# Kernel optimization log

Hardware: AMD Instinct MI355X
Metric: run time of the kernel (lower is better)

## Reference

```python
import jax, jax.numpy as jnp
import numpy as np

# dims
B, S, V, H, D, I, L, SL, P = 1, 2048, 32000, 1024, 512, 4096, 2, 32, 4096
DECAY_FAST, DECAY_SLOW, CONS_RATE, CONS_EVERY = 0.9, 0.99, 0.1, 10


def _ln(x, g, b):
    m = x.mean(-1, keepdims=True)
    v = ((x - m) ** 2).mean(-1, keepdims=True)
    return (x - m) * jax.lax.rsqrt(v + 1e-5) * g + b


def _memory_scan(items, gates, fast0, slow0):
    # items [B,S,D], gates [B,S,SL]; sequential per-timestep memory update
    cons = (jnp.arange(items.shape[1]) % CONS_EVERY) == 0
    def step(carry, x):
        fast, slow = carry
        item, gate, c = x
        fast = DECAY_FAST * fast + gate[:, :, None] * item[:, None, :]
        slow = jnp.where(c, DECAY_SLOW * slow + CONS_RATE * fast, slow)
        fast = jnp.where(c, (1.0 - CONS_RATE) * fast, fast)
        return (fast, slow), None
    (fast, slow), _ = jax.lax.scan(
        step, (fast0, slow0),
        (items.transpose(1, 0, 2), gates.transpose(1, 0, 2), cons))
    return fast, slow


def _forward(input_ids, fast_states, slow_states, emb, pos_emb, W_item, b_item,
             W_q, b_q, rh_W1, rh_b1, rh_W2, rh_b2, gate_W, gate_b, W_out, b_out,
             ln1_g, ln1_b, ffn_W1, ffn_b1, ffn_W2, ffn_b2, ln2_g, ln2_b, fln_g, fln_b):
    b, s = input_ids.shape
    h = emb[input_ids] + pos_emb[:s][None]  # [B,S,H]
    new_fast, new_slow = [], []
    for l in range(W_item.shape[0]):
        items = h @ W_item[l] + b_item[l]          # [B,S,D]
        query = h @ W_q[l] + b_q[l]                # [B,S,H]
        # retrieval head -> unit-norm unbinding keys
        k1 = jax.nn.gelu(items @ rh_W1[l] + rh_b1[l])
        keys = k1 @ rh_W2[l] + rh_b2[l]
        keys = keys / (jnp.linalg.norm(keys, axis=-1, keepdims=True) + 1e-6)
        fast0, slow0 = fast_states[l], slow_states[l]  # [B,SL,D]
        # retrieval uses the initial (constant-within-sequence) states, so it
        # vectorizes over seq: slot attention + hadamard unbinding
        mem = jnp.concatenate([fast0, slow0], axis=1)  # [B,2*SL,D]
        scores = jnp.einsum('bsd,bnd->bsn', keys, mem) / jnp.sqrt(jnp.float32(D))
        attn = jax.nn.softmax(scores, axis=-1)
        retrieved = jnp.einsum('bsn,bnd->bsd', attn, mem) * keys  # [B,S,D]
        gates = jax.nn.sigmoid(jnp.concatenate([h, retrieved], -1) @ gate_W[l] + gate_b[l])
        fast_gates = gates[..., :SL]
        fast, slow = _memory_scan(items, fast_gates, fast0, slow0)
        new_fast.append(fast)
        new_slow.append(slow)
        out = jnp.concatenate([query, retrieved], -1) @ W_out[l] + b_out[l]
        h = _ln(h + out, ln1_g[l], ln1_b[l])
        ffn = jax.nn.gelu(h @ ffn_W1[l] + ffn_b1[l]) @ ffn_W2[l] + ffn_b2[l]
        h = _ln(h + ffn, ln2_g[l], ln2_b[l])
    h = _ln(h, fln_g, fln_b)
    logits = jnp.einsum('bsh,vh->bsv', h, emb)  # tied lm_head
    return logits, jnp.stack(new_fast), jnp.stack(new_slow)


def setup_inputs() -> dict:
    key = jax.random.key(0)
    def rn(i, shape, scale=0.02):
        return jax.random.normal(jax.random.fold_in(key, i), shape, dtype=jnp.float32) * scale
    z = lambda shape: jnp.zeros(shape, jnp.float32)
    return dict(
        input_ids=jax.random.randint(jax.random.fold_in(key, 0), (B, S), 0, V),
        fast_states=rn(100, (L, B, SL, D), 0.5),
        slow_states=rn(101, (L, B, SL, D), 0.5),
        emb=rn(1, (V, H)),
        pos_emb=rn(2, (P, H)),
        W_item=rn(3, (L, H, D)), b_item=z((L, D)),
        W_q=rn(4, (L, H, H)), b_q=z((L, H)),
        rh_W1=rn(5, (L, D, 2 * D)), rh_b1=z((L, 2 * D)),
        rh_W2=rn(6, (L, 2 * D, D)), rh_b2=z((L, D)),
        gate_W=rn(7, (L, H + D, 2 * SL)), gate_b=z((L, 2 * SL)),
        W_out=rn(8, (L, H + D, H)), b_out=z((L, H)),
        ln1_g=jnp.ones((L, H)), ln1_b=z((L, H)),
        ffn_W1=rn(9, (L, H, I)), ffn_b1=z((L, I)),
        ffn_W2=rn(10, (L, I, H)), ffn_b2=z((L, H)),
        ln2_g=jnp.ones((L, H)), ln2_b=z((L, H)),
        fln_g=jnp.ones((H,)), fln_b=z((H,)),
    )


def reference(input_ids, fast_states, slow_states, emb, pos_emb, W_item, b_item,
              W_q, b_q, rh_W1, rh_b1, rh_W2, rh_b2, gate_W, gate_b, W_out, b_out,
              ln1_g, ln1_b, ffn_W1, ffn_b1, ffn_W2, ffn_b2, ln2_g, ln2_b, fln_g, fln_b):
    return _forward(input_ids, fast_states, slow_states, emb, pos_emb, W_item, b_item,
                    W_q, b_q, rh_W1, rh_b1, rh_W2, rh_b2, gate_W, gate_b, W_out, b_out,
                    ln1_g, ln1_b, ffn_W1, ffn_b1, ffn_W2, ffn_b2, ln2_g, ln2_b, fln_g, fln_b)
```

## Files before the change

### kernel.cpp

```cpp
#include <hip/hip_runtime.h>
#include <hip/hip_bf16.h>
#include <stdint.h>

typedef __hip_bfloat16 bf16;
typedef float f32x4 __attribute__((ext_vector_type(4)));
typedef short s16x8 __attribute__((ext_vector_type(8)));
typedef short s16x4 __attribute__((ext_vector_type(4)));

#define DEV __device__ __forceinline__

static constexpr int S_ = 2048, H_ = 1024, D_ = 512, I_ = 4096, V_ = 32000;
static constexpr int SLn = 32, Lc = 2;
static constexpr size_t LOGITS_N = (size_t)S_ * V_;

DEV float gelu_f(float x) {
    float x3 = x * x * x;
    return 0.5f * x * (1.f + tanhf(0.7978845608028654f * (x + 0.044715f * x3)));
}

#define AS1(p) ((const __attribute__((address_space(1))) void*)(uintptr_t)(p))
#define AS3(p) ((__attribute__((address_space(3))) void*)(uint32_t)(uintptr_t)(p))

__global__ __launch_bounds__(256, 2) void logits_gemm(const bf16* __restrict__ A,
                                                      const bf16* __restrict__ BT,
                                                      float* __restrict__ C) {
    constexpr int NT = 32, SLOT = 128 * 32;
    __shared__ short lds[4 * SLOT];
    const int tid = threadIdx.x, lane = tid & 63;
    const int wm = (tid >> 6) >> 1, wn = (tid >> 6) & 1;

    int bid = blockIdx.x;
    int wgid = (bid & 7) * 250 + (bid >> 3);
    const int m0 = (wgid & 7) * 256;
    const int n0 = (wgid >> 3) * 128;

    const bf16* bS[2];
#pragma unroll
    for (int c = 0; c < 2; ++c) {
        int L = (c * 256 + tid) * 16;
        int sidx = L >> 10, w = L & 1023;
        int r16 = w >> 6;
        int c2 = (w & 63) ^ (((r16 >> 3) & 1) << 5);
        bS[c] = BT + (size_t)(n0 + sidx * 16 + r16) * 1024 + (c2 >> 1);
    }
    auto stageB = [&](int kt) {
        short* dst = &lds[(kt & 3) * SLOT];
#pragma unroll
        for (int c = 0; c < 2; ++c)
            __builtin_amdgcn_global_load_lds(AS1(bS[c] + kt * 32), AS3(dst + (c * 256 + tid) * 8), 16, 0, 0);
    };
    const int laneoff = ((lane & 15) * 64 + ((((lane >> 4) * 8) ^ (((lane >> 3) & 1) << 4)) << 1)) >> 1;

    const bf16* aP[8];
#pragma unroll
    for (int fi = 0; fi < 8; ++fi)
        aP[fi] = A + (size_t)(m0 + wm * 128 + fi * 16 + (lane & 15)) * 1536 + ((lane >> 4) * 8);

    f32x4 acc[8][4];
#pragma unroll
    for (int i = 0; i < 8; i++)
#pragma unroll
        for (int j = 0; j < 4; j++)
#pragma unroll
            for (int r = 0; r < 4; r++) acc[i][j][r] = 0.f;

    s16x8 a0[8], a1[8];
    stageB(0);
    stageB(1);
    stageB(2);
#pragma unroll
    for (int fi = 0; fi < 8; ++fi) a0[fi] = *(const s16x8*)(aP[fi]);
    asm volatile("s_waitcnt vmcnt(0)" ::: "memory");
    __builtin_amdgcn_s_barrier();

    auto iter = [&](int t, s16x8(&cur)[8], s16x8(&nxt)[8]) {
        const short* bs = &lds[(t & 3) * SLOT];
        s16x8 bf[4];
#pragma unroll
        for (int j = 0; j < 4; ++j)
            bf[j] = *(const s16x8*)&bs[(wn * 4 + j) * 512 + laneoff];
        if (t + 1 < NT) {
#pragma unroll
            for (int fi = 0; fi < 8; ++fi) nxt[fi] = *(const s16x8*)(aP[fi] + (t + 1) * 32);
        }
        if (t >= 1 && t + 2 < NT) stageB(t + 2);
        if (t + 2 < NT)
            asm volatile("s_waitcnt vmcnt(10)" ::: "memory");
        else if (t + 1 < NT)
            asm volatile("s_waitcnt vmcnt(8)" ::: "memory");
        else
            asm volatile("s_waitcnt vmcnt(0)" ::: "memory");
        asm volatile("s_waitcnt lgkmcnt(0)" ::: "memory");
        __builtin_amdgcn_s_barrier();
        __builtin_amdgcn_sched_barrier(0);
        __builtin_amdgcn_s_setprio(1);
#pragma unroll
        for (int i = 0; i < 8; ++i)
#pragma unroll
            for (int j = 0; j < 4; ++j)
                acc[i][j] = __builtin_amdgcn_mfma_f32_16x16x32_bf16(cur[i], bf[j], acc[i][j], 0, 0, 0);
        __builtin_amdgcn_s_setprio(0);
    };

    for (int t = 0; t < NT; t += 2) {
        iter(t, a0, a1);
        iter(t + 1, a1, a0);
    }

#pragma unroll
    for (int i = 0; i < 8; i++) {
        int gr0 = m0 + (wm * 8 + i) * 16 + ((lane >> 4) << 2);
#pragma unroll
        for (int j = 0; j < 4; j++) {
            int gc = n0 + (wn * 4 + j) * 16 + (lane & 15);
#pragma unroll
            for (int r = 0; r < 4; r++) C[(size_t)(gr0 + r) * V_ + gc] = acc[i][j][r];
        }
    }
}

template <int BM, int BN, int TH, int WM, int WN, int FLAGS>
__global__ __launch_bounds__(TH, 3) void gemm_p5(
    const bf16* __restrict__ A, int lda, const bf16* __restrict__ BT,
    const float* __restrict__ bias, const float* __restrict__ bias2,
    float* __restrict__ Cf, int ldf, bf16* __restrict__ Cb, int ldb2,
    bf16* __restrict__ Cb2, int K, int Mt, int Nt) {
    constexpr int FM = BM / (WM * 16), FN = BN / (WN * 16);
    constexpr int CA = (BM * 4) / TH, CB = (BN * 4) / TH, CH = CA + CB;
    constexpr int NPH = (FM * FN >= 32) ? 2 : 1;
    constexpr int FMP = FM / NPH;
    constexpr int BUFS = (BM + BN) * 32;
    __shared__ short lds[4 * BUFS];
    const int tid = threadIdx.x, lane = tid & 63;
    const int wm = (tid >> 6) / WN, wn = (tid >> 6) % WN;

    int nwg = Mt * Nt;
    int bid = blockIdx.x, wgid = bid;
    if ((nwg & 7) == 0) {
        int cpx = nwg >> 3;
        wgid = (bid & 7) * cpx + (bid >> 3);
    }
    const int m0 = (wgid % Mt) * BM, n0 = (wgid / Mt) * BN;

    const bf16* aS[CA];
    const bf16* bS[CB];
#pragma unroll
    for (int c = 0; c < CA; ++c) {
        int L = (c * TH + tid) * 16;
        int sidx = L >> 10, w = L & 1023;
        int r16 = w >> 6;
        int c2 = (w & 63) ^ (((r16 >> 3) & 1) << 5);
        aS[c] = A + (size_t)(m0 + sidx * 16 + r16) * lda + (c2 >> 1);
    }
#pragma unroll
    for (int c = 0; c < CB; ++c) {
        int L = (c * TH + tid) * 16;
        int sidx = L >> 10, w = L & 1023;
        int r16 = w >> 6;
        int c2 = (w & 63) ^ (((r16 >> 3) & 1) << 5);
        bS[c] = BT + (size_t)(n0 + sidx * 16 + r16) * K + (c2 >> 1);
    }

    auto stageA = [&](int kt) {
        short* dst = &lds[(kt & 3) * BUFS];
#pragma unroll
        for (int c = 0; c < CA; ++c)
            __builtin_amdgcn_global_load_lds(AS1(aS[c] + kt * 32), AS3(dst + (c * TH + tid) * 8), 16, 0, 0);
    };
    auto stageB = [&](int kt) {
        short* dst = &lds[(kt & 3) * BUFS + BM * 32];
#pragma unroll
        for (int c = 0; c < CB; ++c)
            __builtin_amdgcn_global_load_lds(AS1(bS[c] + kt * 32), AS3(dst + (c * TH + tid) * 8), 16, 0, 0);
    };

    const int laneoff = ((lane & 15) * 64 + ((((lane >> 4) * 8) ^ (((lane >> 3) & 1) << 4)) << 1)) >> 1;

    f32x4 acc[FM][FN];
#pragma unroll
    for (int i = 0; i < FM; i++)
#pragma unroll
        for (int j = 0; j < FN; j++)
#pragma unroll
            for (int r = 0; r < 4; r++) acc[i][j][r] = 0.f;

    const int NT = K >> 5;
    stageA(0); stageB(0);
    stageA(1); stageB(1);
    stageA(2); stageB(2);
    asm volatile("s_waitcnt vmcnt(%0)" ::"n"(2 * CH) : "memory");
    __builtin_amdgcn_s_barrier();
    for (int t = 0; t < NT; ++t) {
        const short* as = &lds[(t & 3) * BUFS];
        const short* bs = as + BM * 32;
        s16x8 bf[FN];
#pragma unroll
        for (int p = 0; p < NPH; ++p) {
            s16x8 af[FMP];
#pragma unroll
            for (int i = 0; i < FMP; i++)
                af[i] = *(const s16x8*)&as[(wm * FM + p * FMP + i) * 512 + laneoff];
            if (p == 0) {
#pragma unroll
                for (int j = 0; j < FN; j++)
                    bf[j] = *(const s16x8*)&bs[(wn * FN + j) * 512 + laneoff];
            }
            if (t + 3 < NT) {
                if (NPH == 1) {
                    stageA(t + 3);
                    stageB(t + 3);
                } else if (p == 0) {
                    stageA(t + 3);
                } else {
                    stageB(t + 3);
                }
            }
            if (p == NPH - 1) {
                const int rem = NT - 1 - t;
                if (rem >= 3)
                    asm volatile("s_waitcnt vmcnt(%0)" ::"n"(2 * CH) : "memory");
                else if (rem == 2)
                    asm volatile("s_waitcnt vmcnt(%0)" ::"n"(CH) : "memory");
                else
                    asm volatile("s_waitcnt vmcnt(0)" ::: "memory");
            }
            __builtin_amdgcn_s_barrier();
            __builtin_amdgcn_sched_barrier(0);
            __builtin_amdgcn_s_setprio(1);
#pragma unroll
            for (int i = 0; i < FMP; i++)
#pragma unroll
                for (int j = 0; j < FN; j++)
                    acc[p * FMP + i][j] =
                        __builtin_amdgcn_mfma_f32_16x16x32_bf16(af[i], bf[j], acc[p * FMP + i][j], 0, 0, 0);
            __builtin_amdgcn_s_setprio(0);
            __builtin_amdgcn_s_barrier();
        }
    }

#pragma unroll
    for (int i = 0; i < FM; i++) {
        int gr0 = m0 + (wm * FM + i) * 16 + ((lane >> 4) << 2);
#pragma unroll
        for (int j = 0; j < FN; j++) {
            int gc = n0 + (wn * FN + j) * 16 + (lane & 15);
            if (FLAGS & 32) {
                if (n0 < 512) {
                    float bv = bias[gc];
#pragma unroll
                    for (int r = 0; r < 4; r++) {
                        float v = acc[i][j][r] + bv;
                        Cf[(size_t)(gr0 + r) * 512 + gc] = v;
                        Cb2[(size_t)(gr0 + r) * 512 + gc] = __float2bfloat16(v);
                    }
                } else {
                    float bv = bias2[gc - 512];
#pragma unroll
                    for (int r = 0; r < 4; r++)
                        Cb[(size_t)(gr0 + r) * 1536 + (gc - 512)] = __float2bfloat16(acc[i][j][r] + bv);
                }
            } else {
                float bv = (FLAGS & 1) ? bias[gc] : 0.f;
#pragma unroll
                for (int r = 0; r < 4; r++) {
                    float v = acc[i][j][r] + bv;
                    if (FLAGS & 2) v = gelu_f(v);
                    if (FLAGS & 4) Cf[(size_t)(gr0 + r) * ldf + gc] = v;
                    if (FLAGS & 8) Cb[(size_t)(gr0 + r) * ldb2 + gc] = __float2bfloat16(v);
                }
            }
        }
    }
}

__global__ __launch_bounds__(256) void transpose_bf16_kernel(const float* __restrict__ W,
                                                             bf16* __restrict__ WT, int K, int N) {
    __shared__ float t[32][33];
    int tx = threadIdx.x & 31, ty = threadIdx.x >> 5;
    int kb = blockIdx.y * 32, nb = blockIdx.x * 32;
#pragma unroll
    for (int i = 0; i < 4; i++)
        t[ty + 8 * i][tx] = W[(size_t)(kb + ty + 8 * i) * N + nb + tx];
    __syncthreads();
#pragma unroll
    for (int i = 0; i < 4; i++)
        WT[(size_t)(nb + ty + 8 * i) * K + kb + tx] = __float2bfloat16(t[tx][ty + 8 * i]);
}

__global__ void conv_bf16_kernel(const float* __restrict__ src, bf16* __restrict__ dst) {
    size_t i = (size_t)blockIdx.x * 256 + threadIdx.x;
    f32x4 v = ((const f32x4*)src)[i];
    s16x4 o;
#pragma unroll
    for (int j = 0; j < 4; j++) {
        bf16 h = __float2bfloat16(v[j]);
        o[j] = *(short*)&h;
    }
    ((s16x4*)dst)[i] = o;
}

__global__ void embed_kernel(const int* __restrict__ ids, const float* __restrict__ emb,
                             const float* __restrict__ pos, float* __restrict__ hF,
                             bf16* __restrict__ hB) {
    int t = blockIdx.x, tid = threadIdx.x;
    int id = ids[t];
    f32x4 v = ((const f32x4*)(emb + (size_t)id * H_))[tid];
    f32x4 q = ((const f32x4*)(pos + (size_t)t * H_))[tid];
    v = v + q;
    ((f32x4*)(hF + (size_t)t * H_))[tid] = v;
    s16x4 o;
#pragma unroll
    for (int j = 0; j < 4; j++) {
        bf16 h = __float2bfloat16(v[j]);
        o[j] = *(short*)&h;
    }
    ((s16x4*)(hB + (size_t)t * 1536))[tid] = o;
}

__global__ __launch_bounds__(256) void ln_kernel(const float* __restrict__ x,
                                                 const float* __restrict__ res,
                                                 const float* __restrict__ g,
                                                 const float* __restrict__ b,
                                                 float* __restrict__ of, bf16* __restrict__ ob,
                                                 int ldo) {
    __shared__ float red[8];
    int row = blockIdx.x, tid = threadIdx.x, lane = tid & 63, wid = tid >> 6;
    const float* xr = x + (size_t)row * H_;
    float v[4];
#pragma unroll
    for (int j = 0; j < 4; j++) {
        int c = tid + 256 * j;
        v[j] = xr[c] + (res ? res[(size_t)row * H_ + c] : 0.f);
    }
    float s = v[0] + v[1] + v[2] + v[3];
#pragma unroll
    for (int o = 32; o; o >>= 1) s += __shfl_xor(s, o);
    if (!lane) red[wid] = s;
    __syncthreads();
    float mean = (red[0] + red[1] + red[2] + red[3]) * (1.f / H_);
    float q = 0.f;
#pragma unroll
    for (int j = 0; j < 4; j++) {
        float d = v[j] - mean;
        q += d * d;
    }
#pragma unroll
    for (int o = 32; o; o >>= 1) q += __shfl_xor(q, o);
    if (!lane) red[4 + wid] = q;
    __syncthreads();
    float var = (red[4] + red[5] + red[6] + red[7]) * (1.f / H_);
    float rstd = rsqrtf(var + 1e-5f);
#pragma unroll
    for (int j = 0; j < 4; j++) {
        int c = tid + 256 * j;
        float o2 = (v[j] - mean) * rstd * g[c] + b[c];
        if (of) of[(size_t)row * H_ + c] = o2;
        if (ob) ob[(size_t)row * ldo + c] = __float2bfloat16(o2);
    }
}

__global__ void memt_kernel(const float* __restrict__ fast0, const float* __restrict__ slow0,
                            float* __restrict__ memT) {
    int idx = blockIdx.x * 256 + threadIdx.x;
    int d = idx >> 6, n = idx & 63;
    const float* m = (n < 32) ? fast0 + (size_t)n * D_ : slow0 + (size_t)(n - 32) * D_;
    memT[idx] = m[d];
}

__global__ __launch_bounds__(256) void attn_kernel(const float* __restrict__ keys,
                                                   const float* __restrict__ memT,
                                                   const float* __restrict__ fast0,
                                                   const float* __restrict__ slow0,
                                                   bf16* __restrict__ qr, bf16* __restrict__ hr) {
    __shared__ float klds[4][512];
    int wid = threadIdx.x >> 6, lane = threadIdx.x & 63;
    int r = blockIdx.x * 4 + wid;
    float kv[8], ss = 0.f;
#pragma unroll
    for (int j = 0; j < 8; j++) {
        kv[j] = keys[(size_t)r * D_ + lane + 64 * j];
        ss += kv[j] * kv[j];
    }
#pragma unroll
    for (int o = 32; o; o >>= 1) ss += __shfl_xor(ss, o);
    float inv = 1.f / (sqrtf(ss) + 1e-6f);
#pragma unroll
    for (int j = 0; j < 8; j++) {
        kv[j] *= inv;
        klds[wid][lane + 64 * j] = kv[j];
    }
    __syncthreads();
    float s0 = 0.f, s1 = 0.f, s2 = 0.f, s3 = 0.f;
#pragma unroll 8
    for (int d = 0; d < 512; d += 4) {
        s0 = fmaf(klds[wid][d + 0], memT[(d + 0) * 64 + lane], s0);
        s1 = fmaf(klds[wid][d + 1], memT[(d + 1) * 64 + lane], s1);
        s2 = fmaf(klds[wid][d + 2], memT[(d + 2) * 64 + lane], s2);
        s3 = fmaf(klds[wid][d + 3], memT[(d + 3) * 64 + lane], s3);
    }
    float s = (s0 + s1 + s2 + s3) * 0.044194173824159216f;
    float m = s;
#pragma unroll
    for (int o = 32; o; o >>= 1) m = fmaxf(m, __shfl_xor(m, o));
    float p = expf(s - m);
    float sum = p;
#pragma unroll
    for (int o = 32; o; o >>= 1) sum += __shfl_xor(sum, o);
    float pn = p / sum;
    float rv[8];
#pragma unroll
    for (int j = 0; j < 8; j++) rv[j] = 0.f;
    for (int n2 = 0; n2 < 64; ++n2) {
        float a2 = __shfl(pn, n2);
        const float* m2 = (n2 < 32) ? (fast0 + (size_t)n2 * D_) : (slow0 + (size_t)(n2 - 32) * D_);
#pragma unroll
        for (int j = 0; j < 8; j++) rv[j] = fmaf(a2, m2[lane + 64 * j], rv[j]);
    }
#pragma unroll
    for (int j = 0; j < 8; j++) {
        bf16 o = __float2bfloat16(rv[j] * kv[j]);
        qr[(size_t)r * 1536 + 1024 + lane + 64 * j] = o;
        hr[(size_t)r * 1536 + 1024 + lane + 64 * j] = o;
    }
}

__global__ void coef_kernel(float* __restrict__ coef) {
    int t = blockIdx.x * 256 + threadIdx.x;
    int j0 = (t + 9) / 10;
    float a = powf(0.9f, (float)(2047 - t + 205 - j0));
    float b = 0.f;
    for (int j = j0; j < 205; ++j)
        b += powf(0.9f, (float)(10 * j - t + j - j0)) * powf(0.99f, (float)(204 - j));
    b *= 0.1f;
    coef[t] = a;
    coef[2048 + t] = b;
    if (t == 0) {
        coef[4096] = powf(0.99f, 205.f);
        float cfs = 0.f;
        for (int j = 0; j < 205; ++j)
            cfs += powf(0.9f, (float)(11 * j + 1)) * powf(0.99f, (float)(204 - j));
        coef[4097] = 0.1f * cfs;
    }
}

__global__ void sigcoef_kernel(const float* __restrict__ raw, const float* __restrict__ coef,
                               float* __restrict__ ga, float* __restrict__ gb) {
    int i = blockIdx.x * 256 + threadIdx.x;
    int r = i >> 5, n = i & 31;
    float g = 1.f / (1.f + expf(-raw[r * 64 + n]));
    ga[i] = g * coef[r];
    gb[i] = g * coef[2048 + r];
}

__global__ __launch_bounds__(256) void scan_part_kernel(const float* __restrict__ items,
                                                        const float* __restrict__ ga,
                                                        const float* __restrict__ gb,
                                                        float* __restrict__ pF,
                                                        float* __restrict__ pS) {
    int tid = threadIdx.x;
    int d = (blockIdx.x & 7) * 64 + (tid & 63);
    int mg = (blockIdx.x >> 3) & 1;
    int tc = blockIdx.x >> 4;
    int m0 = mg * 16 + (tid >> 6) * 4;
    float aF[4] = {0.f, 0.f, 0.f, 0.f}, aS[4] = {0.f, 0.f, 0.f, 0.f};
    for (int t = tc * 128; t < tc * 128 + 128; ++t) {
        float it = items[(size_t)t * D_ + d];
#pragma unroll
        for (int j = 0; j < 4; j++) {
            aF[j] = fmaf(ga[t * 32 + m0 + j], it, aF[j]);
            aS[j] = fmaf(gb[t * 32 + m0 + j], it, aS[j]);
        }
    }
#pragma unroll
    for (int j = 0; j < 4; j++) {
        pF[((size_t)tc * 32 + m0 + j) * D_ + d] = aF[j];
        pS[((size_t)tc * 32 + m0 + j) * D_ + d] = aS[j];
    }
}

__global__ __launch_bounds__(256) void scan_reduce_kernel(const float* __restrict__ pF,
                                                          const float* __restrict__ pS,
                                                          const float* __restrict__ coef,
                                                          const float* __restrict__ fast0,
                                                          const float* __restrict__ slow0,
                                                          float* __restrict__ fastO,
                                                          float* __restrict__ slowO) {
    int i = blockIdx.x * 256 + threadIdx.x;
    float f = 0.f, s = 0.f;
#pragma unroll
    for (int c = 0; c < 16; c++) {
        f += pF[(size_t)c * 32 * D_ + i];
        s += pS[(size_t)c * 32 * D_ + i];
    }
    fastO[i] = f;
    slowO[i] = s + coef[4096] * slow0[i] + coef[4097] * fast0[i];
}

static inline void gemmM(hipStream_t st, const bf16* A, int lda, const bf16* BT,
                         const float* bias, const float* bias2, float* Cf, int ldf, bf16* Cb,
                         int ldb2, bf16* Cb2, int M, int N, int K, int flags) {
    int Mt = M / 128, Nt = N / 64;
    dim3 g(Mt * Nt), b(256);
#define GCASE(fl)                                                                                  \
    if (flags == fl) {                                                                             \
        gemm_p5<128, 64, 256, 2, 2, fl><<<g, b, 0, st>>>(A, lda, BT, bias, bias2, Cf, ldf, Cb,     \
                                                         ldb2, Cb2, K, Mt, Nt);                    \
        return;                                                                                    \
    }
    GCASE(33)
    GCASE(11)
    GCASE(5)
#undef GCASE
}

static inline void transp(hipStream_t st, const float* W, bf16* WT, int K, int N) {
    transpose_bf16_kernel<<<dim3(N / 32, K / 32), 256, 0, st>>>(W, WT, K, N);
}

extern "C" void kernel_launch(void* const* d_in, const int* in_sizes, int n_in,
                              void* d_out, int out_size, void* d_ws, size_t ws_size,
                              hipStream_t stream) {
    const int* ids = (const int*)d_in[0];
    const float* fastS = (const float*)d_in[1];
    const float* slowS = (const float*)d_in[2];
    const float* emb = (const float*)d_in[3];
    const float* pos = (const float*)d_in[4];
    const float* W_item = (const float*)d_in[5];
    const float* b_item = (const float*)d_in[6];
    const float* W_q = (const float*)d_in[7];
    const float* b_q = (const float*)d_in[8];
    const float* rh_W1 = (const float*)d_in[9];
    const float* rh_b1 = (const float*)d_in[10];
    const float* rh_W2 = (const float*)d_in[11];
    const float* rh_b2 = (const float*)d_in[12];
    const float* gate_W = (const float*)d_in[13];
    const float* gate_b = (const float*)d_in[14];
    const float* W_out = (const float*)d_in[15];
    const float* b_out = (const float*)d_in[16];
    const float* ln1_g = (const float*)d_in[17];
    const float* ln1_b = (const float*)d_in[18];
    const float* ffn_W1 = (const float*)d_in[19];
    const float* ffn_b1 = (const float*)d_in[20];
    const float* ffn_W2 = (const float*)d_in[21];
    const float* ffn_b2 = (const float*)d_in[22];
    const float* ln2_g = (const float*)d_in[23];
    const float* ln2_b = (const float*)d_in[24];
    const float* fln_g = (const float*)d_in[25];
    const float* fln_b = (const float*)d_in[26];
    float* outP = (float*)d_out;

    size_t off = 0;
    char* base = (char*)d_ws;
    auto alloc = [&](size_t n) -> char* {
        char* p = base + off;
        off += (n + 255) & ~(size_t)255;
        return p;
    };
    bf16* wIQ = (bf16*)alloc((size_t)Lc * 1536 * H_ * 2);
    bf16* rh1T = (bf16*)alloc((size_t)Lc * (2 * D_) * D_ * 2);
    bf16* rh2T = (bf16*)alloc((size_t)Lc * D_ * (2 * D_) * 2);
    bf16* wOutT = (bf16*)alloc((size_t)Lc * H_ * 1536 * 2);
    bf16* f1T = (bf16*)alloc((size_t)Lc * I_ * H_ * 2);
    bf16* f2T = (bf16*)alloc((size_t)Lc * H_ * I_ * 2);
    bf16* gWT = (bf16*)alloc((size_t)Lc * 64 * 1536 * 2);
    bf16* embB = (bf16*)alloc((size_t)V_ * H_ * 2);
    float* hF = (float*)alloc((size_t)S_ * H_ * 4);
    bf16* hrB = (bf16*)alloc((size_t)S_ * 1536 * 2);
    bf16* hB = hrB;
    float* itemsF = (float*)alloc((size_t)S_ * D_ * 4);
    bf16* itemsB = (bf16*)alloc((size_t)S_ * D_ * 2);
    bf16* qrB = (bf16*)alloc((size_t)S_ * 1536 * 2);
    bf16* k1B = (bf16*)alloc((size_t)S_ * (2 * D_) * 2);
    float* keysF = (float*)alloc((size_t)S_ * D_ * 4);
    float* outF = (float*)alloc((size_t)S_ * H_ * 4);
    bf16* ffn1B = (bf16*)alloc((size_t)S_ * I_ * 2);
    float* gRawF = (float*)alloc((size_t)S_ * 64 * 4);
    float* gaF = (float*)alloc((size_t)S_ * SLn * 4);
    float* gbF = (float*)alloc((size_t)S_ * SLn * 4);
    float* coefF = (float*)alloc(4200 * 4);
    float* memT = (float*)alloc((size_t)D_ * 64 * 4);
    float* pF = (float*)alloc((size_t)16 * SLn * D_ * 4);
    float* pS = (float*)alloc((size_t)16 * SLn * D_ * 4);

    coef_kernel<<<8, 256, 0, stream>>>(coefF);
    for (int l = 0; l < Lc; ++l) {
        transp(stream, W_item + (size_t)l * H_ * D_, wIQ + (size_t)l * 1536 * H_, H_, D_);
        transp(stream, W_q + (size_t)l * H_ * H_, wIQ + (size_t)l * 1536 * H_ + (size_t)512 * H_,
               H_, H_);
        transp(stream, rh_W1 + (size_t)l * D_ * 2 * D_, rh1T + (size_t)l * 2 * D_ * D_, D_, 2 * D_);
        transp(stream, rh_W2 + (size_t)l * 2 * D_ * D_, rh2T + (size_t)l * D_ * 2 * D_, 2 * D_, D_);
        transp(stream, W_out + (size_t)l * 1536 * H_, wOutT + (size_t)l * H_ * 1536, 1536, H_);
        transp(stream, ffn_W1 + (size_t)l * H_ * I_, f1T + (size_t)l * I_ * H_, H_, I_);
        transp(stream, ffn_W2 + (size_t)l * I_ * H_, f2T + (size_t)l * H_ * I_, I_, H_);
        transp(stream, gate_W + (size_t)l * 1536 * 64, gWT + (size_t)l * 64 * 1536, 1536, 64);
    }
    conv_bf16_kernel<<<(int)((size_t)V_ * H_ / 4 / 256), 256, 0, stream>>>(emb, embB);
    embed_kernel<<<S_, 256, 0, stream>>>(ids, emb, pos, hF, hB);

    for (int l = 0; l < Lc; ++l) {
        const float* fast0 = fastS + (size_t)l * SLn * D_;
        const float* slow0 = slowS + (size_t)l * SLn * D_;
        gemmM(stream, hB, 1536, wIQ + (size_t)l * 1536 * H_, b_item + l * D_, b_q + l * H_,
              itemsF, 512, qrB, 1536, itemsB, S_, 1536, H_, 33);
        gemmM(stream, itemsB, D_, rh1T + (size_t)l * 2 * D_ * D_, rh_b1 + l * 2 * D_, nullptr,
              nullptr, 0, k1B, 2 * D_, nullptr, S_, 2 * D_, D_, 11);
        gemmM(stream, k1B, 2 * D_, rh2T + (size_t)l * D_ * 2 * D_, rh_b2 + l * D_, nullptr,
              keysF, D_, nullptr, 0, nullptr, S_, D_, 2 * D_, 5);
        memt_kernel<<<128, 256, 0, stream>>>(fast0, slow0, memT);
        attn_kernel<<<S_ / 4, 256, 0, stream>>>(keysF, memT, fast0, slow0, qrB, hrB);
        gemmM(stream, hrB, 1536, gWT + (size_t)l * 64 * 1536, gate_b + l * 64, nullptr, gRawF,
              64, nullptr, 0, nullptr, S_, 64, 1536, 5);
        sigcoef_kernel<<<S_ * SLn / 256, 256, 0, stream>>>(gRawF, coefF, gaF, gbF);
        scan_part_kernel<<<256, 256, 0, stream>>>(itemsF, gaF, gbF, pF, pS);
        scan_reduce_kernel<<<64, 256, 0, stream>>>(
            pF, pS, coefF, fast0, slow0, outP + LOGITS_N + (size_t)l * SLn * D_,
            outP + LOGITS_N + (size_t)Lc * SLn * D_ + (size_t)l * SLn * D_);
        gemmM(stream, qrB, 1536, wOutT + (size_t)l * H_ * 1536, b_out + l * H_, nullptr, outF,
              H_, nullptr, 0, nullptr, S_, H_, 1536, 5);
        ln_kernel<<<S_, 256, 0, stream>>>(hF, outF, ln1_g + l * H_, ln1_b + l * H_, hF, hB, 1536);
        gemmM(stream, hB, 1536, f1T + (size_t)l * I_ * H_, ffn_b1 + l * I_, nullptr, nullptr, 0,
              ffn1B, I_, nullptr, S_, I_, H_, 11);
        gemmM(stream, ffn1B, I_, f2T + (size_t)l * H_ * I_, ffn_b2 + l * H_, nullptr, outF, H_,
              nullptr, 0, nullptr, S_, H_, I_, 5);
        ln_kernel<<<S_, 256, 0, stream>>>(hF, outF, ln2_g + l * H_, ln2_b + l * H_, hF, hB, 1536);
    }
    ln_kernel<<<S_, 256, 0, stream>>>(hF, nullptr, fln_g, fln_b, nullptr, hB, 1536);
    logits_gemm<<<2000, 256, 0, stream>>>(hB, embB, outP);
}
```

Before: 1.031 ms.

## Restructure logits GEMM into 256x256 eight-wave tiles with staged LDS pipeline

The logits GEMM moves from 256x128 tiles with 4 waves, where A is read straight from global memory into registers, to 256x256 tiles with 8 waves. Both A and B are now staged into a 128KB double-buffered LDS through global_load_lds, and the loop is split into eight quarter-phases that interleave LDS reads, async loads and MFMA blocks. Separately, GEMMs with N>=1536 now use a 128x128 tile instead of 128x64, and the split-output epilogue is changed to test by column so it stays correct with wider tiles. This is meant to raise data reuse per tile and overlap memory with compute, at the cost of one block per CU, higher register pressure and more barriers.

```diff
diff --git a/kernel.cpp b/kernel.cpp
--- a/kernel.cpp
+++ b/kernel.cpp
@@ -21,41 +21,50 @@
 #define AS1(p) ((const __attribute__((address_space(1))) void*)(uintptr_t)(p))
 #define AS3(p) ((__attribute__((address_space(3))) void*)(uint32_t)(uintptr_t)(p))
 
-__global__ __launch_bounds__(256, 2) void logits_gemm(const bf16* __restrict__ A,
-                                                      const bf16* __restrict__ BT,
-                                                      float* __restrict__ C) {
-    constexpr int NT = 32, SLOT = 128 * 32;
-    __shared__ short lds[4 * SLOT];
+__global__ __launch_bounds__(512, 1) void logits_gemm8(const bf16* __restrict__ A,
+                                                       const bf16* __restrict__ BT,
+                                                       float* __restrict__ C) {
+    constexpr int NT = 16, NI = 8;
+    __shared__ short lds[65536];
     const int tid = threadIdx.x, lane = tid & 63;
-    const int wm = (tid >> 6) >> 1, wn = (tid >> 6) & 1;
+    const int wid = tid >> 6;
+    const int wm = wid >> 2, wn = wid & 3;
 
     int bid = blockIdx.x;
-    int wgid = (bid & 7) * 250 + (bid >> 3);
+    int wgid = (bid & 7) * 125 + (bid >> 3);
     const int m0 = (wgid & 7) * 256;
-    const int n0 = (wgid >> 3) * 128;
-
-    const bf16* bS[2];
+    const int n0 = (wgid >> 3) * 256;
+
+    const bf16* aB[2];
+    const bf16* bB[2];
 #pragma unroll
     for (int c = 0; c < 2; ++c) {
-        int L = (c * 256 + tid) * 16;
+        int L = (c * 512 + tid) * 16;
         int sidx = L >> 10, w = L & 1023;
         int r16 = w >> 6;
         int c2 = (w & 63) ^ (((r16 >> 3) & 1) << 5);
-        bS[c] = BT + (size_t)(n0 + sidx * 16 + r16) * 1024 + (c2 >> 1);
-    }
-    auto stageB = [&](int kt) {
-        short* dst = &lds[(kt & 3) * SLOT];
+        int row = (sidx >> 1) * 16 + r16;
+        int col = ((sidx & 1) * 64 + c2) >> 1;
+        aB[c] = A + (size_t)(m0 + row) * 1536 + col;
+        bB[c] = BT + (size_t)(n0 + row) * 1024 + col;
+    }
+    auto STA = [&](int d, int h, int kt) {
 #pragma unroll
         for (int c = 0; c < 2; ++c)
-            __builtin_amdgcn_global_load_lds(AS1(bS[c] + kt * 32), AS3(dst + (c * 256 + tid) * 8), 16, 0, 0);
-    };
+            __builtin_amdgcn_global_load_lds(AS1(aB[c] + (size_t)h * 196608 + kt * 64),
+                                             AS3(&lds[d * 32768 + h * 8192 + (c * 512 + tid) * 8]),
+                                             16, 0, 0);
+    };
+    auto STB = [&](int d, int h, int kt) {
+#pragma unroll
+        for (int c = 0; c < 2; ++c)
+            __builtin_amdgcn_global_load_lds(AS1(bB[c] + (size_t)h * 131072 + kt * 64),
+                                             AS3(&lds[d * 32768 + 16384 + h * 8192 + (c * 512 + tid) * 8]),
+                                             16, 0, 0);
+    };
+
     const int laneoff = ((lane & 15) * 64 + ((((lane >> 4) * 8) ^ (((lane >> 3) & 1) << 4)) << 1)) >> 1;
 
-    const bf16* aP[8];
-#pragma unroll
-    for (int fi = 0; fi < 8; ++fi)
-        aP[fi] = A + (size_t)(m0 + wm * 128 + fi * 16 + (lane & 15)) * 1536 + ((lane >> 4) * 8);
-
     f32x4 acc[8][4];
 #pragma unroll
     for (int i = 0; i < 8; i++)
@@ -64,55 +73,95 @@
 #pragma unroll
             for (int r = 0; r < 4; r++) acc[i][j][r] = 0.f;
 
-    s16x8 a0[8], a1[8];
-    stageB(0);
-    stageB(1);
-    stageB(2);
-#pragma unroll
-    for (int fi = 0; fi < 8; ++fi) a0[fi] = *(const s16x8*)(aP[fi]);
-    asm volatile("s_waitcnt vmcnt(0)" ::: "memory");
+    s16x8 aq[4][2], b0r[2][2], b1r[2][2];
+    auto rdA = [&](int d, int mq) {
+        const short* p = &lds[d * 32768 + wm * 8192 + mq * 4096];
+#pragma unroll
+        for (int f = 0; f < 4; ++f)
+#pragma unroll
+            for (int ks = 0; ks < 2; ++ks)
+                aq[f][ks] = *(const s16x8*)&p[(f * 2 + ks) * 512 + laneoff];
+    };
+    auto rdB0 = [&](int d, int nq) {
+        const short* p = &lds[d * 32768 + 16384 + (wn >> 1) * 8192 + (wn & 1) * 4096 + nq * 2048];
+#pragma unroll
+        for (int g = 0; g < 2; ++g)
+#pragma unroll
+            for (int ks = 0; ks < 2; ++ks)
+                b0r[g][ks] = *(const s16x8*)&p[(g * 2 + ks) * 512 + laneoff];
+    };
+    auto rdB1 = [&](int d, int nq) {
+        const short* p = &lds[d * 32768 + 16384 + (wn >> 1) * 8192 + (wn & 1) * 4096 + nq * 2048];
+#pragma unroll
+        for (int g = 0; g < 2; ++g)
+#pragma unroll
+            for (int ks = 0; ks < 2; ++ks)
+                b1r[g][ks] = *(const s16x8*)&p[(g * 2 + ks) * 512 + laneoff];
+    };
+
+#define PHASE_SYNC()                                     \
+    __builtin_amdgcn_s_barrier();                        \
+    asm volatile("s_waitcnt lgkmcnt(0)" ::: "memory");   \
+    __builtin_amdgcn_sched_barrier(0)
+#define MMQ(mq, nq, B)                                                                         \
+    do {                                                                                       \
+        __builtin_amdgcn_s_setprio(1);                                                         \
+        _Pragma("unroll") for (int f = 0; f < 4; ++f)                                          \
+            _Pragma("unroll") for (int g = 0; g < 2; ++g)                                      \
+                _Pragma("unroll") for (int ks = 0; ks < 2; ++ks)                               \
+                    acc[(mq)*4 + f][(nq)*2 + g] = __builtin_amdgcn_mfma_f32_16x16x32_bf16(     \
+                        aq[f][ks], B[g][ks], acc[(mq)*4 + f][(nq)*2 + g], 0, 0, 0);            \
+        __builtin_amdgcn_s_setprio(0);                                                         \
+        __builtin_amdgcn_s_barrier();                                                          \
+    } while (0)
+
+    STA(0, 0, 0); STA(0, 1, 0); STB(0, 0, 0); STB(0, 1, 0);
+    STB(1, 0, 1); STA(1, 0, 1);
+    asm volatile("s_waitcnt vmcnt(4)" ::: "memory");
     __builtin_amdgcn_s_barrier();
 
-    auto iter = [&](int t, s16x8(&cur)[8], s16x8(&nxt)[8]) {
-        const short* bs = &lds[(t & 3) * SLOT];
-        s16x8 bf[4];
-#pragma unroll
-        for (int j = 0; j < 4; ++j)
-            bf[j] = *(const s16x8*)&bs[(wn * 4 + j) * 512 + laneoff];
-        if (t + 1 < NT) {
-#pragma unroll
-            for (int fi = 0; fi < 8; ++fi) nxt[fi] = *(const s16x8*)(aP[fi] + (t + 1) * 32);
+    for (int it = 0; it < NI; ++it) {
+        const int k0 = 2 * it, k1 = k0 + 1;
+        const bool s0 = (k0 + 2 < NT);
+        const bool s1 = (k1 + 2 < NT);
+        rdA(0, 0); rdB0(0, 0);
+        STA(1, 1, k1);
+        PHASE_SYNC(); MMQ(0, 0, b0r);
+        rdB1(0, 1);
+        STB(1, 1, k1);
+        PHASE_SYNC(); MMQ(0, 1, b1r);
+        rdA(0, 1);
+        if (s0) STB(0, 0, k0 + 2);
+        PHASE_SYNC(); MMQ(1, 0, b0r);
+        if (s0) {
+            STA(0, 0, k0 + 2);
+            asm volatile("s_waitcnt vmcnt(4)" ::: "memory");
+        } else {
+            asm volatile("s_waitcnt vmcnt(0)" ::: "memory");
         }
-        if (t >= 1 && t + 2 < NT) stageB(t + 2);
-        if (t + 2 < NT)
-            asm volatile("s_waitcnt vmcnt(10)" ::: "memory");
-        else if (t + 1 < NT)
-            asm volatile("s_waitcnt vmcnt(8)" ::: "memory");
-        else
-            asm volatile("s_waitcnt vmcnt(0)" ::: "memory");
-        asm volatile("s_waitcnt lgkmcnt(0)" ::: "memory");
-        __builtin_amdgcn_s_barrier();
-        __builtin_amdgcn_sched_barrier(0);
-        __builtin_amdgcn_s_setprio(1);
-#pragma unroll
-        for (int i = 0; i < 8; ++i)
-#pragma unroll
-            for (int j = 0; j < 4; ++j)
-                acc[i][j] = __builtin_amdgcn_mfma_f32_16x16x32_bf16(cur[i], bf[j], acc[i][j], 0, 0, 0);
-        __builtin_amdgcn_s_setprio(0);
-    };
-
-    for (int t = 0; t < NT; t += 2) {
-        iter(t, a0, a1);
-        iter(t + 1, a1, a0);
-    }
+        PHASE_SYNC(); MMQ(1, 1, b1r);
+        rdA(1, 0); rdB0(1, 0);
+        if (s0) STA(0, 1, k0 + 2);
+        PHASE_SYNC(); MMQ(0, 0, b0r);
+        rdB1(1, 1);
+        if (s0) STB(0, 1, k0 + 2);
+        PHASE_SYNC(); MMQ(0, 1, b1r);
+        rdA(1, 1);
+        if (s1) STB(1, 0, k1 + 2);
+        PHASE_SYNC(); MMQ(1, 0, b0r);
+        if (s1) STA(1, 0, k1 + 2);
+        if (it < NI - 1) asm volatile("s_waitcnt vmcnt(4)" ::: "memory");
+        PHASE_SYNC(); MMQ(1, 1, b1r);
+    }
+#undef PHASE_SYNC
+#undef MMQ
 
 #pragma unroll
     for (int i = 0; i < 8; i++) {
-        int gr0 = m0 + (wm * 8 + i) * 16 + ((lane >> 4) << 2);
+        int gr0 = m0 + wm * 128 + i * 16 + ((lane >> 4) << 2);
 #pragma unroll
         for (int j = 0; j < 4; j++) {
-            int gc = n0 + (wn * 4 + j) * 16 + (lane & 15);
+            int gc = n0 + wn * 64 + j * 16 + (lane & 15);
 #pragma unroll
             for (int r = 0; r < 4; r++) C[(size_t)(gr0 + r) * V_ + gc] = acc[i][j][r];
         }
@@ -245,7 +294,7 @@
         for (int j = 0; j < FN; j++) {
             int gc = n0 + (wn * FN + j) * 16 + (lane & 15);
             if (FLAGS & 32) {
-                if (n0 < 512) {
+                if (gc < 512) {
                     float bv = bias[gc];
 #pragma unroll
                     for (int r = 0; r < 4; r++) {
@@ -499,18 +548,28 @@
 static inline void gemmM(hipStream_t st, const bf16* A, int lda, const bf16* BT,
                          const float* bias, const float* bias2, float* Cf, int ldf, bf16* Cb,
                          int ldb2, bf16* Cb2, int M, int N, int K, int flags) {
+    if (N >= 1536 && (N % 128) == 0) {
+        int Mt = M / 128, Nt = N / 128;
+        dim3 g(Mt * Nt), b(256);
+        if (flags == 33)
+            gemm_p5<128, 128, 256, 2, 2, 33><<<g, b, 0, st>>>(A, lda, BT, bias, bias2, Cf, ldf,
+                                                              Cb, ldb2, Cb2, K, Mt, Nt);
+        else if (flags == 11)
+            gemm_p5<128, 128, 256, 2, 2, 11><<<g, b, 0, st>>>(A, lda, BT, bias, bias2, Cf, ldf,
+                                                              Cb, ldb2, Cb2, K, Mt, Nt);
+        else
+            gemm_p5<128, 128, 256, 2, 2, 5><<<g, b, 0, st>>>(A, lda, BT, bias, bias2, Cf, ldf,
+                                                             Cb, ldb2, Cb2, K, Mt, Nt);
+        return;
+    }
     int Mt = M / 128, Nt = N / 64;
     dim3 g(Mt * Nt), b(256);
-#define GCASE(fl)                                                                                  \
-    if (flags == fl) {                                                                             \
-        gemm_p5<128, 64, 256, 2, 2, fl><<<g, b, 0, st>>>(A, lda, BT, bias, bias2, Cf, ldf, Cb,     \
-                                                         ldb2, Cb2, K, Mt, Nt);                    \
-        return;                                                                                    \
-    }
-    GCASE(33)
-    GCASE(11)
-    GCASE(5)
-#undef GCASE
+    if (flags == 11)
+        gemm_p5<128, 64, 256, 2, 2, 11><<<g, b, 0, st>>>(A, lda, BT, bias, bias2, Cf, ldf, Cb,
+                                                         ldb2, Cb2, K, Mt, Nt);
+    else
+        gemm_p5<128, 64, 256, 2, 2, 5><<<g, b, 0, st>>>(A, lda, BT, bias, bias2, Cf, ldf, Cb,
+                                                        ldb2, Cb2, K, Mt, Nt);
 }
 
 static inline void transp(hipStream_t st, const float* W, bf16* WT, int K, int N) {
@@ -625,5 +684,5 @@
         ln_kernel<<<S_, 256, 0, stream>>>(hF, outF, ln2_g + l * H_, ln2_b + l * H_, hF, hB, 1536);
     }
     ln_kernel<<<S_, 256, 0, stream>>>(hF, nullptr, fln_g, fln_b, nullptr, hB, 1536);
-    logits_gemm<<<2000, 256, 0, stream>>>(hB, embB, outP);
-}
+    logits_gemm8<<<1000, 512, 0, stream>>>(hB, embB, outP);
+}
```

Result: faster. 889.8 us (-13.7%).

## Enlarge logits GEMM tile to 256x256 with LDS-staged A and B

Applied to the files above, without the earlier changes.

The logits GEMM moves from 256x128 tiles with 4 waves to 256x256 tiles with 8 waves. Both A and B are now staged into LDS through global_load_lds with a 4-slot ring buffer, where before A was read straight from global memory into registers. Each K step is split into two half-steps so LDS reads overlap the MFMAs. Separately, the generic GEMM helper now uses 128x128 tiles for wide N (at least 1536), which means the gc<512 split in the flag-33 epilogue has to be checked per column instead of per tile. The goal is more data reuse per loaded byte and less global traffic, paid for with one block per CU, more LDS use and higher register pressure.

```diff
diff --git a/kernel.cpp b/kernel.cpp
--- a/kernel.cpp
+++ b/kernel.cpp
@@ -21,40 +21,43 @@
 #define AS1(p) ((const __attribute__((address_space(1))) void*)(uintptr_t)(p))
 #define AS3(p) ((__attribute__((address_space(3))) void*)(uint32_t)(uintptr_t)(p))
 
-__global__ __launch_bounds__(256, 2) void logits_gemm(const bf16* __restrict__ A,
+__global__ __launch_bounds__(512, 1) void logits_gemm(const bf16* __restrict__ A,
                                                       const bf16* __restrict__ BT,
                                                       float* __restrict__ C) {
-    constexpr int NT = 32, SLOT = 128 * 32;
-    __shared__ short lds[4 * SLOT];
+    constexpr int NT = 32;
+    __shared__ short lds[4 * 16384];
     const int tid = threadIdx.x, lane = tid & 63;
-    const int wm = (tid >> 6) >> 1, wn = (tid >> 6) & 1;
+    const int wid = tid >> 6;
+    const int wm = wid >> 2, wn = wid & 3;
 
     int bid = blockIdx.x;
-    int wgid = (bid & 7) * 250 + (bid >> 3);
+    int wgid = (bid & 7) * 125 + (bid >> 3);
     const int m0 = (wgid & 7) * 256;
-    const int n0 = (wgid >> 3) * 128;
-
-    const bf16* bS[2];
-#pragma unroll
-    for (int c = 0; c < 2; ++c) {
-        int L = (c * 256 + tid) * 16;
-        int sidx = L >> 10, w = L & 1023;
-        int r16 = w >> 6;
-        int c2 = (w & 63) ^ (((r16 >> 3) & 1) << 5);
-        bS[c] = BT + (size_t)(n0 + sidx * 16 + r16) * 1024 + (c2 >> 1);
-    }
-    auto stageB = [&](int kt) {
-        short* dst = &lds[(kt & 3) * SLOT];
-#pragma unroll
-        for (int c = 0; c < 2; ++c)
-            __builtin_amdgcn_global_load_lds(AS1(bS[c] + kt * 32), AS3(dst + (c * 256 + tid) * 8), 16, 0, 0);
-    };
-    const int laneoff = ((lane & 15) * 64 + ((((lane >> 4) * 8) ^ (((lane >> 3) & 1) << 4)) << 1)) >> 1;
-
-    const bf16* aP[8];
-#pragma unroll
-    for (int fi = 0; fi < 8; ++fi)
-        aP[fi] = A + (size_t)(m0 + wm * 128 + fi * 16 + (lane & 15)) * 1536 + ((lane >> 4) * 8);
+    const int n0 = (wgid >> 3) * 256;
+
+    const int L = tid * 16;
+    const int sidx = L >> 10, w = L & 1023;
+    const int r16 = w >> 6;
+    const int c2 = (w & 63) ^ (((r16 >> 3) & 1) << 5);
+    const int srow = sidx * 16 + r16;
+    const int scol = c2 >> 1;
+    const bf16* aSrc[2];
+    const bf16* bSrc[2];
+#pragma unroll
+    for (int h = 0; h < 2; ++h) {
+        aSrc[h] = A + (size_t)(m0 + h * 128 + srow) * 1536 + scol;
+        bSrc[h] = BT + (size_t)(n0 + h * 128 + srow) * 1024 + scol;
+    }
+    auto STA = [&](int kt, int h) {
+        __builtin_amdgcn_global_load_lds(AS1(aSrc[h] + kt * 32),
+                                         AS3(&lds[(kt & 3) * 16384 + h * 4096 + tid * 8]), 16, 0, 0);
+    };
+    auto STB = [&](int kt, int h) {
+        __builtin_amdgcn_global_load_lds(AS1(bSrc[h] + kt * 32),
+                                         AS3(&lds[(kt & 3) * 16384 + 8192 + h * 4096 + tid * 8]), 16, 0, 0);
+    };
+
+    const int laneoff = (lane & 15) * 32 + (((lane >> 4) * 8) ^ (((lane >> 3) & 1) << 4));
 
     f32x4 acc[8][4];
 #pragma unroll
@@ -64,55 +67,86 @@
 #pragma unroll
             for (int r = 0; r < 4; r++) acc[i][j][r] = 0.f;
 
-    s16x8 a0[8], a1[8];
-    stageB(0);
-    stageB(1);
-    stageB(2);
-#pragma unroll
-    for (int fi = 0; fi < 8; ++fi) a0[fi] = *(const s16x8*)(aP[fi]);
-    asm volatile("s_waitcnt vmcnt(0)" ::: "memory");
+    s16x8 a0[4], a1[4], b0[4], b1[4];
+    auto rdA = [&](s16x8(&d)[4], int kt, int mq) {
+        const short* p = &lds[(kt & 3) * 16384 + wm * 4096 + mq * 2048];
+#pragma unroll
+        for (int f = 0; f < 4; ++f) d[f] = *(const s16x8*)&p[f * 512 + laneoff];
+    };
+    auto rdB = [&](s16x8(&d)[4], int kt) {
+        const short* p = &lds[(kt & 3) * 16384 + 8192 + wn * 2048];
+#pragma unroll
+        for (int j = 0; j < 4; ++j) d[j] = *(const s16x8*)&p[j * 512 + laneoff];
+    };
+    auto MM = [&](int mq, s16x8(&a)[4], s16x8(&b)[4]) {
+        __builtin_amdgcn_s_setprio(1);
+#pragma unroll
+        for (int f = 0; f < 4; ++f)
+#pragma unroll
+            for (int j = 0; j < 4; ++j)
+                acc[mq * 4 + f][j] =
+                    __builtin_amdgcn_mfma_f32_16x16x32_bf16(a[f], b[j], acc[mq * 4 + f][j], 0, 0, 0);
+        __builtin_amdgcn_s_setprio(0);
+    };
+
+#define GATE(tight)                                                     \
+    do {                                                                \
+        __builtin_amdgcn_s_barrier();                                   \
+        if (tight) asm volatile("s_waitcnt vmcnt(0)" ::: "memory");     \
+        else       asm volatile("s_waitcnt vmcnt(4)" ::: "memory");     \
+        asm volatile("s_waitcnt lgkmcnt(0)" ::: "memory");              \
+        __builtin_amdgcn_sched_barrier(0);                              \
+    } while (0)
+#define SB() __builtin_amdgcn_sched_barrier(0)
+
+#pragma unroll
+    for (int kt = 0; kt < 3; ++kt) {
+        STA(kt, 0); STA(kt, 1); STB(kt, 0); STB(kt, 1);
+    }
+    asm volatile("s_waitcnt vmcnt(4)" ::: "memory");
     __builtin_amdgcn_s_barrier();
-
-    auto iter = [&](int t, s16x8(&cur)[8], s16x8(&nxt)[8]) {
-        const short* bs = &lds[(t & 3) * SLOT];
-        s16x8 bf[4];
-#pragma unroll
-        for (int j = 0; j < 4; ++j)
-            bf[j] = *(const s16x8*)&bs[(wn * 4 + j) * 512 + laneoff];
-        if (t + 1 < NT) {
-#pragma unroll
-            for (int fi = 0; fi < 8; ++fi) nxt[fi] = *(const s16x8*)(aP[fi] + (t + 1) * 32);
+    rdA(a0, 0, 0);
+    rdB(b0, 0);
+
+    for (int tt = 0; tt < NT; tt += 2) {
+        {
+            const int t = tt;
+            const bool tight = (t >= NT - 2);
+            GATE(tight);
+            rdA(a1, t, 1);
+            SB();
+            MM(0, a0, b0);
+            if (t + 3 < NT) { STA(t + 3, 0); STA(t + 3, 1); }
+            GATE(tight);
+            if (t + 1 < NT) { rdA(a0, t + 1, 0); rdB(b1, t + 1); }
+            SB();
+            MM(1, a1, b0);
+            if (t + 3 < NT) { STB(t + 3, 0); STB(t + 3, 1); }
         }
-        if (t >= 1 && t + 2 < NT) stageB(t + 2);
-        if (t + 2 < NT)
-            asm volatile("s_waitcnt vmcnt(10)" ::: "memory");
-        else if (t + 1 < NT)
-            asm volatile("s_waitcnt vmcnt(8)" ::: "memory");
-        else
-            asm volatile("s_waitcnt vmcnt(0)" ::: "memory");
-        asm volatile("s_waitcnt lgkmcnt(0)" ::: "memory");
-        __builtin_amdgcn_s_barrier();
-        __builtin_amdgcn_sched_barrier(0);
-        __builtin_amdgcn_s_setprio(1);
-#pragma unroll
-        for (int i = 0; i < 8; ++i)
-#pragma unroll
-            for (int j = 0; j < 4; ++j)
-                acc[i][j] = __builtin_amdgcn_mfma_f32_16x16x32_bf16(cur[i], bf[j], acc[i][j], 0, 0, 0);
-        __builtin_amdgcn_s_setprio(0);
-    };
-
-    for (int t = 0; t < NT; t += 2) {
-        iter(t, a0, a1);
-        iter(t + 1, a1, a0);
-    }
+        {
+            const int t = tt + 1;
+            const bool tight = (t >= NT - 2);
+            GATE(tight);
+            rdA(a1, t, 1);
+            SB();
+            MM(0, a0, b1);
+            if (t + 3 < NT) { STA(t + 3, 0); STA(t + 3, 1); }
+            GATE(tight);
+            if (t + 1 < NT) { rdA(a0, t + 1, 0); rdB(b0, t + 1); }
+            SB();
+            MM(1, a1, b1);
+            if (t + 3 < NT) { STB(t + 3, 0); STB(t + 3, 1); }
+        }
+    }
+#undef GATE
+#undef SB
 
 #pragma unroll
     for (int i = 0; i < 8; i++) {
-        int gr0 = m0 + (wm * 8 + i) * 16 + ((lane >> 4) << 2);
+        int gr0 = m0 + wm * 128 + i * 16 + ((lane >> 4) << 2);
 #pragma unroll
         for (int j = 0; j < 4; j++) {
-            int gc = n0 + (wn * 4 + j) * 16 + (lane & 15);
+            int gc = n0 + wn * 64 + j * 16 + (lane & 15);
 #pragma unroll
             for (int r = 0; r < 4; r++) C[(size_t)(gr0 + r) * V_ + gc] = acc[i][j][r];
         }
@@ -245,7 +279,7 @@
         for (int j = 0; j < FN; j++) {
             int gc = n0 + (wn * FN + j) * 16 + (lane & 15);
             if (FLAGS & 32) {
-                if (n0 < 512) {
+                if (gc < 512) {
                     float bv = bias[gc];
 #pragma unroll
                     for (int r = 0; r < 4; r++) {
@@ -499,18 +533,28 @@
 static inline void gemmM(hipStream_t st, const bf16* A, int lda, const bf16* BT,
                          const float* bias, const float* bias2, float* Cf, int ldf, bf16* Cb,
                          int ldb2, bf16* Cb2, int M, int N, int K, int flags) {
+    if (N >= 1536 && (N % 128) == 0) {
+        int Mt = M / 128, Nt = N / 128;
+        dim3 g(Mt * Nt), b(256);
+        if (flags == 33)
+            gemm_p5<128, 128, 256, 2, 2, 33><<<g, b, 0, st>>>(A, lda, BT, bias, bias2, Cf, ldf,
+                                                              Cb, ldb2, Cb2, K, Mt, Nt);
+        else if (flags == 11)
+            gemm_p5<128, 128, 256, 2, 2, 11><<<g, b, 0, st>>>(A, lda, BT, bias, bias2, Cf, ldf,
+                                                              Cb, ldb2, Cb2, K, Mt, Nt);
+        else
+            gemm_p5<128, 128, 256, 2, 2, 5><<<g, b, 0, st>>>(A, lda, BT, bias, bias2, Cf, ldf,
+                                                             Cb, ldb2, Cb2, K, Mt, Nt);
+        return;
+    }
     int Mt = M / 128, Nt = N / 64;
     dim3 g(Mt * Nt), b(256);
-#define GCASE(fl)                                                                                  \
-    if (flags == fl) {                                                                             \
-        gemm_p5<128, 64, 256, 2, 2, fl><<<g, b, 0, st>>>(A, lda, BT, bias, bias2, Cf, ldf, Cb,     \
-                                                         ldb2, Cb2, K, Mt, Nt);                    \
-        return;                                                                                    \
-    }
-    GCASE(33)
-    GCASE(11)
-    GCASE(5)
-#undef GCASE
+    if (flags == 11)
+        gemm_p5<128, 64, 256, 2, 2, 11><<<g, b, 0, st>>>(A, lda, BT, bias, bias2, Cf, ldf, Cb,
+                                                         ldb2, Cb2, K, Mt, Nt);
+    else
+        gemm_p5<128, 64, 256, 2, 2, 5><<<g, b, 0, st>>>(A, lda, BT, bias, bias2, Cf, ldf, Cb,
+                                                        ldb2, Cb2, K, Mt, Nt);
 }
 
 static inline void transp(hipStream_t st, const float* W, bf16* WT, int K, int N) {
@@ -625,5 +669,5 @@
         ln_kernel<<<S_, 256, 0, stream>>>(hF, outF, ln2_g + l * H_, ln2_b + l * H_, hF, hB, 1536);
     }
     ln_kernel<<<S_, 256, 0, stream>>>(hF, nullptr, fln_g, fln_b, nullptr, hB, 1536);
-    logits_gemm<<<2000, 256, 0, stream>>>(hB, embB, outP);
-}
+    logits_gemm<<<1000, 512, 0, stream>>>(hB, embB, outP);
+}
```

Measured after the change: 887.6 us (median of 3 runs). -13.9%, faster.
